# Kernel tuning notes

Hardware: AMD Instinct MI355X
Metric: run time of the kernel (lower is better)

Reference implementation:

```python
import jax, jax.numpy as jnp
import numpy as np

PI = 3.141592653589793
DET_THRESHOLD = 0.25
MAX_DET = 100
REG_HEAD = 4
DEPTH_MEAN = 28.01  # smoke_coder.depth_ref[0]
DIM_REF = (3.88, 1.63, 1.53)  # smoke_coder.dim_ref[0] (l, h, w)


def setup_inputs() -> dict:
    key = jax.random.key(0)
    k1, k2, k3, k4 = jax.random.split(key, 4)
    B, C, H, W = 32, 3, 256, 832  # stride-4 feature map of 3328x1024 images
    pred_heatmap = jax.random.uniform(k1, (B, C, H, W), dtype=jnp.float32)
    pred_regression = jax.random.normal(k2, (B, C + 1, H, W), dtype=jnp.float32) * 0.1  # REG_HEAD=4 channels
    trans_mat = jnp.tile(jnp.array([[0.25, 0.0, 0.0], [0.0, 0.25, 0.0], [0.0, 0.0, 1.0]], jnp.float32), (B, 1, 1))
    K_mat = jnp.tile(jnp.array([[2100.0, 0.0, 1664.0], [0.0, 2100.0, 512.0], [0.0, 0.0, 1.0]], jnp.float32), (B, 1, 1))
    size = jnp.tile(jnp.array([3328.0, 1024.0], jnp.float32), (B, 1))  # (img_w, img_h)
    h_cam = jax.random.uniform(k3, (B,), jnp.float32, 1.4, 2.0)
    dimensions = jax.random.uniform(k4, (B, 3), jnp.float32, 1.5, 4.0)
    return dict(pred_heatmap=pred_heatmap, pred_regression=pred_regression, trans_mat=trans_mat,
                K_mat=K_mat, size=size, h_cam=h_cam, dimensions=dimensions)


def reference(pred_heatmap, pred_regression, trans_mat, K_mat, size, h_cam, dimensions):
    B, C, H, W = pred_heatmap.shape
    K = MAX_DET
    # ---- nms_hm: 3x3 max-pool, keep local maxima ----
    hmax = jax.lax.reduce_window(pred_heatmap, -jnp.inf, jax.lax.max, (1, 1, 3, 3), (1, 1, 1, 1), 'SAME')
    heat = pred_heatmap * (hmax == pred_heatmap).astype(pred_heatmap.dtype)
    # ---- select_topk: per-class topk then global topk ----
    scores_c, inds_c = jax.lax.top_k(heat.reshape(B, C, H * W), K)  # [B,C,K]
    ys_c = (inds_c // W).astype(jnp.float32)
    xs_c = (inds_c % W).astype(jnp.float32)
    scores, topk_ind = jax.lax.top_k(scores_c.reshape(B, C * K), K)  # [B,K]
    clses = (topk_ind // K).astype(jnp.float32)
    inds = jnp.take_along_axis(inds_c.reshape(B, C * K), topk_ind, axis=1)
    ys = jnp.take_along_axis(ys_c.reshape(B, C * K), topk_ind, axis=1)
    xs = jnp.take_along_axis(xs_c.reshape(B, C * K), topk_ind, axis=1)
    feat = pred_regression.reshape(B, REG_HEAD, H * W).transpose(0, 2, 1)  # [B,HW,R]
    pois = jnp.take_along_axis(feat, inds[:, :, None], axis=1).reshape(-1, REG_HEAD)  # [B*K,R]
    log_dv_delta = pois[:, 0]
    off_u = pois[:, 1]
    ori = pois[:, 2:]
    # ---- feature points -> image points via inverse affine ----
    pts = jnp.stack([xs.reshape(-1), ys.reshape(-1)], axis=1)
    pts = pts + jnp.stack([off_u, jnp.zeros_like(off_u)], axis=1)
    pts_h = jnp.concatenate([pts, jnp.ones((pts.shape[0], 1), pts.dtype)], axis=1)  # [N,3]
    obj = jnp.repeat(jnp.arange(B), K)
    trans_inv = jnp.linalg.inv(trans_mat)[obj]  # [N,3,3]
    img_pts = jnp.einsum('nij,nj->ni', trans_inv, pts_h)[:, :2]
    # ---- per-object camera params ----
    Ks = K_mat[obj]
    h = h_cam[obj]
    kd = dimensions[obj]
    fx, fy, cx = Ks[:, 0, 0], Ks[:, 1, 1], Ks[:, 0, 2]
    dim_ref = jnp.array(DIM_REF, jnp.float32)
    dims = jnp.where(jnp.isfinite(kd), kd, dim_ref[None, :])
    # ---- geometric depth decode ----
    h_ref = h - dims[:, 1] / 2.0
    log_dv_ref = jnp.log(jnp.clip(fy * jnp.abs(h_ref), 1e-7, None) / DEPTH_MEAN)
    log_dv = jnp.clip(log_dv_ref + log_dv_delta, -4.0, 8.0)
    depths = jnp.clip(fy * jnp.abs(h_ref) * jnp.exp(-log_dv), 0.5, 120.0)
    px = (img_pts[:, 0] - cx) * depths / fx
    locs = jnp.stack([px, h, depths], axis=1)  # [N,3]
    # ---- decode_orientation (SMOKE) ----
    rays = jnp.arctan(locs[:, 0] / (locs[:, 2] + 1e-7))
    alphas = jnp.arctan(ori[:, 0] / (ori[:, 1] + 1e-7))
    alphas = alphas + jnp.where(ori[:, 1] >= 0, -PI / 2, PI / 2)
    rotys = alphas + rays
    rotys = jnp.where(rotys > PI, rotys - 2 * PI, rotys)
    rotys = jnp.where(rotys < -PI, rotys + 2 * PI, rotys)
    # ---- encode_box2d: build 3D corners, rotate, project, clamp ----
    cos, sin = jnp.cos(rotys), jnp.sin(rotys)
    cx8 = jnp.array([-0.5, 0.5, 0.5, 0.5, 0.5, -0.5, -0.5, -0.5], jnp.float32)
    cy8 = jnp.array([-1.0, -1.0, 0.0, 0.0, -1.0, -1.0, 0.0, 0.0], jnp.float32)
    cz8 = jnp.array([-0.5, -0.5, -0.5, 0.5, 0.5, 0.5, 0.5, -0.5], jnp.float32)
    xc = dims[:, 0:1] * cx8  # l
    yc = dims[:, 1:2] * cy8  # h
    zc = dims[:, 2:3] * cz8  # w
    bx = cos[:, None] * xc + sin[:, None] * zc
    bz = -sin[:, None] * xc + cos[:, None] * zc
    box3d = jnp.stack([bx, yc, bz], axis=1) + locs[:, :, None]  # [N,3,8]
    proj = jnp.einsum('nij,njk->nik', Ks, box3d)
    uv = proj[:, :2, :] / proj[:, 2:3, :]
    img_w = size.reshape(-1)[0]
    img_h = size.reshape(-1)[1]
    xmins = jnp.clip(jnp.min(uv[:, 0, :], axis=1), 0.0, img_w)
    xmaxs = jnp.clip(jnp.max(uv[:, 0, :], axis=1), 0.0, img_w)
    ymins = jnp.clip(jnp.min(uv[:, 1, :], axis=1), 0.0, img_h)
    ymaxs = jnp.clip(jnp.max(uv[:, 1, :], axis=1), 0.0, img_h)
    box2d = jnp.stack([xmins, ymins, xmaxs, ymaxs], axis=1)
    pred_dims = jnp.roll(dims, -1, axis=1)  # (l,h,w)->(h,w,l)
    result = jnp.concatenate([clses.reshape(-1, 1), alphas[:, None], box2d, pred_dims, locs,
                              rotys[:, None], scores.reshape(-1, 1)], axis=1)  # [N,14]
    # fixed-shape equivalent of boolean filtering: zero out rows below threshold
    keep = (result[:, -1] > DET_THRESHOLD).astype(result.dtype)
    return result * keep[:, None]
```

## Files before the change

### kernel.cpp

```cpp
#include <hip/hip_runtime.h>
#include <math.h>

#define B_ 32
#define C_ 3
#define H_ 256
#define W_ 832
#define HW_ (H_*W_)
#define K_ 100
#define RPB 16
#define PARTS (H_/RPB)
#define NLOAD (W_/4)
#define BLK 256
#define CAP 2048
#define NCAND (C_*PARTS*K_)
#define NB 2048
#define TIE_CAP 128
#define SEL_PASSES 6

typedef unsigned long long ull;

template<int N>
__device__ inline void bitonic_sort_desc(ull* s) {
    for (int k = 2; k <= N; k <<= 1) {
        for (int j = k >> 1; j > 0; j >>= 1) {
            __syncthreads();
            for (int i = threadIdx.x; i < N; i += BLK) {
                int ixj = i ^ j;
                if (ixj > i) {
                    ull a = s[i], b = s[ixj];
                    bool up = ((i & k) == 0);
                    if (up ? (a < b) : (a > b)) { s[i] = b; s[ixj] = a; }
                }
            }
        }
    }
    __syncthreads();
}

__device__ inline void find_digit(const unsigned* __restrict__ hist,
                                  unsigned* __restrict__ wtot,
                                  const int kneed,
                                  int* __restrict__ d_s,
                                  int* __restrict__ krem_s,
                                  int* __restrict__ m_s) {
    const int tid = threadIdx.x;
    const int lane = tid & 63;
    const int wid = tid >> 6;
    unsigned l[8];
    unsigned Ls = 0;
    #pragma unroll
    for (int j = 0; j < 8; ++j) { l[j] = hist[tid * 8 + j]; Ls += l[j]; }
    unsigned x = Ls;
    #pragma unroll
    for (int off = 1; off < 64; off <<= 1) {
        unsigned y = __shfl_down(x, off);
        if (lane + off < 64) x += y;
    }
    if (lane == 0) wtot[wid] = x;
    __syncthreads();
    unsigned tail = 0;
    #pragma unroll
    for (int w = 0; w < 4; ++w) if (w > wid) tail += wtot[w];
    unsigned s = x - Ls + tail;
    #pragma unroll
    for (int j = 7; j >= 0; --j) {
        const unsigned Sj = s + l[j];
        if (Sj >= (unsigned)kneed && s < (unsigned)kneed) {
            *d_s = tid * 8 + j;
            *krem_s = kneed - (int)s;
            *m_s = (int)l[j];
        }
        s = Sj;
    }
    __syncthreads();
}

__device__ inline void select_topk(const ull* __restrict__ buf, const int cnt,
                                   ull* __restrict__ dst,
                                   unsigned* __restrict__ hist,
                                   ull* __restrict__ tie,
                                   unsigned* __restrict__ wtot,
                                   int* __restrict__ sh) {
    const int tid = threadIdx.x;
    if (tid == 0) sh[0] = 0;
    int kneed = K_;
    int pshift = 0;
    ull prefix = 0;
    for (int pass = 0; pass < SEL_PASSES; ++pass) {
        const int rs = 53 - 11 * pass;
        const int shift = (rs > 0) ? rs : 0;
        #pragma unroll
        for (int j = 0; j < NB / BLK; ++j) hist[tid + j * BLK] = 0u;
        if (tid == 0) sh[1] = 0;
        __syncthreads();
        for (int i = tid; i < cnt; i += BLK) {
            const ull key = buf[i];
            if (pass > 0 && (key >> pshift) != prefix) continue;
            atomicAdd(&hist[(unsigned)(key >> shift) & 2047u], 1u);
        }
        __syncthreads();
        find_digit(hist, wtot, kneed, &sh[2], &sh[3], &sh[4]);
        const int d = sh[2], krem = sh[3], m = sh[4];
        const bool last = (m <= TIE_CAP) || (pass == SEL_PASSES - 1);
        for (int i = tid; i < cnt; i += BLK) {
            const ull key = buf[i];
            if (pass > 0 && (key >> pshift) != prefix) continue;
            const int dg = (int)((unsigned)(key >> shift) & 2047u);
            if (dg > d) {
                dst[atomicAdd(&sh[0], 1)] = key;
            } else if (last && dg == d) {
                const int p = atomicAdd(&sh[1], 1);
                if (p < TIE_CAP) tie[p] = key;
            }
        }
        __syncthreads();
        if (last) {
            const int n1 = K_ - krem;
            if (sh[1] <= TIE_CAP) {
                const int mm = sh[1];
                for (int i = tid; i < mm; i += BLK) {
                    const ull key = tie[i];
                    int r = 0;
                    for (int j = 0; j < mm; ++j) r += (tie[j] > key) ? 1 : 0;
                    if (r < krem) dst[n1 + r] = key;
                }
            } else {
                for (int i = tid; i < krem; i += BLK) dst[n1 + i] = tie[0];
            }
            __syncthreads();
            return;
        }
        prefix = (prefix << 11) | (ull)(unsigned)d;
        pshift = shift;
        kneed = krem;
    }
}

__global__ void __launch_bounds__(BLK) topk_part_kernel(
        const float* __restrict__ heat, ull* __restrict__ part_out) {
    const int chan = blockIdx.x / PARTS;
    const int c    = chan % C_;
    const int part = blockIdx.x % PARTS;
    const float* __restrict__ hp = heat + (size_t)chan * HW_;
    const int r0 = part * RPB;
    const int tid = threadIdx.x;
    const bool active = tid < NLOAD;
    const int x4 = tid * 4;
    const int lane = tid & 63;

    __shared__ unsigned hist[NB];
    __shared__ ull buf[CAP];
    __shared__ ull tie[TIE_CAP];
    __shared__ unsigned wtot[4];
    __shared__ int cnt;
    __shared__ int selsh[5];
    if (tid == 0) cnt = 0;

    const bool needL = active && (lane == 0) && (tid > 0);
    const bool needR = active && (lane == 63);

    float4 rA, rB, rC, rD;
    float aL = 0.f, bL = 0.f, cL = 0.f, dL = 0.f;
    float aR = 0.f, bR = 0.f, cR = 0.f, dR = 0.f;
    {
        const int ym1 = (r0 == 0) ? 0 : r0 - 1;
        const int yp1 = (r0 == H_ - 1) ? r0 : r0 + 1;
        if (active) {
            rA = reinterpret_cast<const float4*>(hp + (size_t)ym1 * W_)[tid];
            rB = reinterpret_cast<const float4*>(hp + (size_t)r0  * W_)[tid];
            rC = reinterpret_cast<const float4*>(hp + (size_t)yp1 * W_)[tid];
        }
        if (needL) {
            aL = hp[(size_t)ym1 * W_ + x4 - 1];
            bL = hp[(size_t)r0  * W_ + x4 - 1];
            cL = hp[(size_t)yp1 * W_ + x4 - 1];
        }
        if (needR) {
            aR = hp[(size_t)ym1 * W_ + x4 + 4];
            bR = hp[(size_t)r0  * W_ + x4 + 4];
            cR = hp[(size_t)yp1 * W_ + x4 + 4];
        }
    }
    __syncthreads();

    if (active) {
        for (int r = 0; r < RPB; ++r) {
            const int y = r0 + r;
            const int yn = (y + 2 > H_ - 1) ? H_ - 1 : y + 2;
            rD = reinterpret_cast<const float4*>(hp + (size_t)yn * W_)[tid];
            if (needL) dL = hp[(size_t)yn * W_ + x4 - 1];
            if (needR) dR = hp[(size_t)yn * W_ + x4 + 4];

            float4 vm;
            vm.x = fmaxf(fmaxf(rA.x, rB.x), rC.x);
            vm.y = fmaxf(fmaxf(rA.y, rB.y), rC.y);
            vm.z = fmaxf(fmaxf(rA.z, rB.z), rC.z);
            vm.w = fmaxf(fmaxf(rA.w, rB.w), rC.w);
            const float lmax = needL ? fmaxf(fmaxf(aL, bL), cL) : -INFINITY;
            const float rmax = needR ? fmaxf(fmaxf(aR, bR), cR) : -INFINITY;

            float left  = __shfl_up(vm.w, 1);
            float right = __shfl_down(vm.x, 1);
            if (lane == 0) left = lmax;
            if (lane == 63 || tid == NLOAD - 1) right = rmax;

            const float vn[6] = {left, vm.x, vm.y, vm.z, vm.w, right};
            const float vv[4] = {rB.x, rB.y, rB.z, rB.w};
            #pragma unroll
            for (int i = 0; i < 4; ++i) {
                const float v = vv[i];
                const bool peak = (v >= vn[i]) && (v >= vn[i+1]) && (v >= vn[i+2]);
                const ull m = __ballot(peak);
                if (peak) {
                    const unsigned p = (unsigned)(y * W_ + x4 + i);
                    const unsigned tiek = ((unsigned)c << 18) | p;
                    const ull key = ((ull)__float_as_uint(v) << 32) | (ull)(~tiek);
                    const int rank = __popcll(m & ((1ULL << lane) - 1ULL));
                    const int leader = __ffsll((long long)m) - 1;
                    int base = 0;
                    if (lane == leader) base = atomicAdd(&cnt, (int)__popcll(m));
                    base = __shfl(base, leader);
                    const int pos = base + rank;
                    if (pos < CAP) buf[pos] = key;
                }
            }
            rA = rB; rB = rC; rC = rD;
            aL = bL; bL = cL; cL = dL;
            aR = bR; bR = cR; cR = dR;
        }
    }
    __syncthreads();

    const int cc = (cnt < CAP) ? cnt : CAP;
    ull* o = part_out + (size_t)blockIdx.x * K_;

    if (cc <= K_) {
        for (int i = tid; i < cc; i += BLK) o[i] = buf[i];
        for (int i = cc + tid; i < K_; i += BLK) o[i] = 0ULL;
        return;
    }

    select_topk(buf, cc, o, hist, tie, wtot, selsh);
}

__global__ void __launch_bounds__(BLK) merge_geom_kernel(
        const ull* __restrict__ part_keys, const float* __restrict__ reg,
        const float* __restrict__ trans, const float* __restrict__ Km,
        const float* __restrict__ sz, const float* __restrict__ hcam,
        const float* __restrict__ dimen, float* __restrict__ out) {
    const int b = blockIdx.x;
    const int tid = threadIdx.x;
    __shared__ ull buf[NCAND];
    __shared__ unsigned hist[NB];
    __shared__ ull sel[128];
    __shared__ ull tie[TIE_CAP];
    __shared__ unsigned wtot[4];
    __shared__ int selsh[5];
    const ull* src = part_keys + (size_t)b * NCAND;
    for (int i = tid; i < NCAND; i += BLK) buf[i] = src[i];
    if (tid < 128) sel[tid] = 0ULL;
    __syncthreads();

    select_topk(buf, NCAND, sel, hist, tie, wtot, selsh);

    bitonic_sort_desc<128>(sel);

    for (int i = tid; i < K_; i += BLK) {
        const ull key = sel[i];
        const unsigned tiek = ~(unsigned)(key & 0xFFFFFFFFULL);
        const float score = __uint_as_float((unsigned)(key >> 32));
        const float clsf = (float)((tiek >> 18) & 3u);
        unsigned hw = tiek & 0x3FFFFu;
        if (hw >= HW_) hw = 0;
        const float xs = (float)(hw % W_);
        const float ys = (float)(hw / W_);

        const float* rg = reg + (size_t)b * 4 * HW_;
        const float delta = rg[hw];
        const float off_u = rg[HW_ + hw];
        const float ori0  = rg[2 * HW_ + hw];
        const float ori1  = rg[3 * HW_ + hw];

        const float* T = trans + b * 9;
        const float t00=T[0], t01=T[1], t02=T[2], t10=T[3], t11=T[4], t12=T[5],
                    t20=T[6], t21=T[7], t22=T[8];
        const float det3 = t00*(t11*t22 - t12*t21) - t01*(t10*t22 - t12*t20)
                         + t02*(t10*t21 - t11*t20);
        const float idt = 1.0f / det3;
        const float i00 = (t11*t22 - t12*t21)*idt;
        const float i01 = (t02*t21 - t01*t22)*idt;
        const float i02 = (t01*t12 - t02*t11)*idt;

        const float pu = xs + off_u;
        const float img_x = i00*pu + i01*ys + i02;

        const float* Kb = Km + b * 9;
        const float k00=Kb[0],k01=Kb[1],k02=Kb[2],k10=Kb[3],k11=Kb[4],k12=Kb[5],
                    k20=Kb[6],k21=Kb[7],k22=Kb[8];
        const float fx = k00, fy = k11, cx = k02;
        const float h = hcam[b];
        float d0 = dimen[b*3+0], d1 = dimen[b*3+1], d2 = dimen[b*3+2];
        if (!isfinite(d0)) d0 = 3.88f;
        if (!isfinite(d1)) d1 = 1.63f;
        if (!isfinite(d2)) d2 = 1.53f;

        const float h_ref = h - d1 * 0.5f;
        const float fyh = fy * fabsf(h_ref);
        const float log_dv_ref = logf(fmaxf(fyh, 1e-7f) / 28.01f);
        const float log_dv = fminf(fmaxf(log_dv_ref + delta, -4.0f), 8.0f);
        const float depth = fminf(fmaxf(fyh * expf(-log_dv), 0.5f), 120.0f);
        const float px = (img_x - cx) * depth / fx;

        const float PI_F  = 3.14159265358979323846f;
        const float ray = atanf(px / (depth + 1e-7f));
        float alpha = atanf(ori0 / (ori1 + 1e-7f));
        alpha += (ori1 >= 0.0f) ? -1.5707963267948966f : 1.5707963267948966f;
        float roty = alpha + ray;
        if (roty >  PI_F) roty -= 6.283185307179586f;
        if (roty < -PI_F) roty += 6.283185307179586f;

        const float cosr = cosf(roty), sinr = sinf(roty);
        const float cx8[8] = {-0.5f, 0.5f, 0.5f, 0.5f, 0.5f,-0.5f,-0.5f,-0.5f};
        const float cy8[8] = {-1.0f,-1.0f, 0.0f, 0.0f,-1.0f,-1.0f, 0.0f, 0.0f};
        const float cz8[8] = {-0.5f,-0.5f,-0.5f, 0.5f, 0.5f, 0.5f, 0.5f,-0.5f};
        float umin = 1e30f, umax = -1e30f, vmin = 1e30f, vmax = -1e30f;
        #pragma unroll
        for (int j = 0; j < 8; ++j) {
            const float xc = d0 * cx8[j];
            const float yc = d1 * cy8[j];
            const float zc = d2 * cz8[j];
            const float X = cosr*xc + sinr*zc + px;
            const float Y = yc + h;
            const float Z = -sinr*xc + cosr*zc + depth;
            const float w = k20*X + k21*Y + k22*Z;
            const float u = (k00*X + k01*Y + k02*Z) / w;
            const float v = (k10*X + k11*Y + k12*Z) / w;
            umin = fminf(umin, u); umax = fmaxf(umax, u);
            vmin = fminf(vmin, v); vmax = fmaxf(vmax, v);
        }
        const float img_w = sz[0], img_h = sz[1];
        const float xmin = fminf(fmaxf(umin, 0.0f), img_w);
        const float xmax = fminf(fmaxf(umax, 0.0f), img_w);
        const float ymin = fminf(fmaxf(vmin, 0.0f), img_h);
        const float ymax = fminf(fmaxf(vmax, 0.0f), img_h);

        const float keep = (score > 0.25f) ? 1.0f : 0.0f;
        float* o = out + (size_t)(b * K_ + i) * 14;
        o[0]  = clsf  * keep;
        o[1]  = alpha * keep;
        o[2]  = xmin  * keep;
        o[3]  = ymin  * keep;
        o[4]  = xmax  * keep;
        o[5]  = ymax  * keep;
        o[6]  = d1    * keep;
        o[7]  = d2    * keep;
        o[8]  = d0    * keep;
        o[9]  = px    * keep;
        o[10] = h     * keep;
        o[11] = depth * keep;
        o[12] = roty  * keep;
        o[13] = score * keep;
    }
}

extern "C" void kernel_launch(void* const* d_in, const int* in_sizes, int n_in,
                              void* d_out, int out_size, void* d_ws, size_t ws_size,
                              hipStream_t stream) {
    const float* heat  = (const float*)d_in[0];
    const float* reg   = (const float*)d_in[1];
    const float* trans = (const float*)d_in[2];
    const float* Kmat  = (const float*)d_in[3];
    const float* sz    = (const float*)d_in[4];
    const float* hcam  = (const float*)d_in[5];
    const float* dimen = (const float*)d_in[6];
    float* out = (float*)d_out;

    ull* part_keys = (ull*)d_ws;

    topk_part_kernel<<<B_ * C_ * PARTS, BLK, 0, stream>>>(heat, part_keys);
    merge_geom_kernel<<<B_, BLK, 0, stream>>>(
        part_keys, reg, trans, Kmat, sz, hcam, dimen, out);
}
```

Baseline: 241.4 us.

## Use overlapping wave halos, deeper row prefetch, and aggregated histogram atomics

The 3x3 NMS scan is restructured so that each wave covers 62 quads plus one ghost lane on each side. Neighbour columns then come from shuffles instead of extra scalar halo loads. Rows are kept in a six-deep register ring so that loads run further ahead, and the four per-column ballots are combined into a single atomicAdd per wave per row. The first radix-select pass now groups equal digits within a wave before each shared-memory atomic, to cut contention. In exchange, edge quads are loaded redundantly, more registers are used, and the leader-election loop costs extra when digits are diverse.

```diff
diff --git a/kernel.cpp b/kernel.cpp
--- a/kernel.cpp
+++ b/kernel.cpp
@@ -6,16 +6,17 @@
 #define H_ 256
 #define W_ 832
 #define HW_ (H_*W_)
+#define NQ (W_/4)
 #define K_ 100
 #define RPB 16
 #define PARTS (H_/RPB)
-#define NLOAD (W_/4)
 #define BLK 256
 #define CAP 2048
 #define NCAND (C_*PARTS*K_)
 #define NB 2048
 #define TIE_CAP 128
 #define SEL_PASSES 6
+#define QPW 62
 
 typedef unsigned long long ull;
 
@@ -82,6 +83,7 @@
                                    unsigned* __restrict__ wtot,
                                    int* __restrict__ sh) {
     const int tid = threadIdx.x;
+    const int lane = tid & 63;
     if (tid == 0) sh[0] = 0;
     int kneed = K_;
     int pshift = 0;
@@ -93,10 +95,25 @@
         for (int j = 0; j < NB / BLK; ++j) hist[tid + j * BLK] = 0u;
         if (tid == 0) sh[1] = 0;
         __syncthreads();
-        for (int i = tid; i < cnt; i += BLK) {
-            const ull key = buf[i];
-            if (pass > 0 && (key >> pshift) != prefix) continue;
-            atomicAdd(&hist[(unsigned)(key >> shift) & 2047u], 1u);
+        if (pass == 0) {
+            for (int i = tid; i < cnt; i += BLK) {
+                const unsigned dg = (unsigned)(buf[i] >> shift) & 2047u;
+                ull unclaimed = __ballot(1);
+                while (unclaimed) {
+                    const int leader = __ffsll((long long)unclaimed) - 1;
+                    const unsigned ldg = __shfl(dg, leader);
+                    const ull same = __ballot(dg == ldg);
+                    if (lane == leader)
+                        atomicAdd(&hist[ldg], (unsigned)__popcll(same));
+                    unclaimed &= ~same;
+                }
+            }
+        } else {
+            for (int i = tid; i < cnt; i += BLK) {
+                const ull key = buf[i];
+                if ((key >> pshift) != prefix) continue;
+                atomicAdd(&hist[(unsigned)(key >> shift) & 2047u], 1u);
+            }
         }
         __syncthreads();
         find_digit(hist, wtot, kneed, &sh[2], &sh[3], &sh[4]);
@@ -144,9 +161,13 @@
     const float* __restrict__ hp = heat + (size_t)chan * HW_;
     const int r0 = part * RPB;
     const int tid = threadIdx.x;
-    const bool active = tid < NLOAD;
-    const int x4 = tid * 4;
     const int lane = tid & 63;
+    const int wid = tid >> 6;
+
+    const int q = QPW * wid + lane - 1;
+    const bool ghost = (q < 0) || (q >= NQ);
+    const int qc = (q < 0) ? 0 : ((q >= NQ) ? NQ - 1 : q);
+    const bool emitter = (lane >= 1) && (lane <= QPW) && !ghost;
 
     __shared__ unsigned hist[NB];
     __shared__ ull buf[CAP];
@@ -156,77 +177,64 @@
     __shared__ int selsh[5];
     if (tid == 0) cnt = 0;
 
-    const bool needL = active && (lane == 0) && (tid > 0);
-    const bool needR = active && (lane == 63);
-
-    float4 rA, rB, rC, rD;
-    float aL = 0.f, bL = 0.f, cL = 0.f, dL = 0.f;
-    float aR = 0.f, bR = 0.f, cR = 0.f, dR = 0.f;
-    {
-        const int ym1 = (r0 == 0) ? 0 : r0 - 1;
-        const int yp1 = (r0 == H_ - 1) ? r0 : r0 + 1;
-        if (active) {
-            rA = reinterpret_cast<const float4*>(hp + (size_t)ym1 * W_)[tid];
-            rB = reinterpret_cast<const float4*>(hp + (size_t)r0  * W_)[tid];
-            rC = reinterpret_cast<const float4*>(hp + (size_t)yp1 * W_)[tid];
-        }
-        if (needL) {
-            aL = hp[(size_t)ym1 * W_ + x4 - 1];
-            bL = hp[(size_t)r0  * W_ + x4 - 1];
-            cL = hp[(size_t)yp1 * W_ + x4 - 1];
-        }
-        if (needR) {
-            aR = hp[(size_t)ym1 * W_ + x4 + 4];
-            bR = hp[(size_t)r0  * W_ + x4 + 4];
-            cR = hp[(size_t)yp1 * W_ + x4 + 4];
-        }
-    }
-    __syncthreads();
-
-    if (active) {
-        for (int r = 0; r < RPB; ++r) {
-            const int y = r0 + r;
-            const int yn = (y + 2 > H_ - 1) ? H_ - 1 : y + 2;
-            rD = reinterpret_cast<const float4*>(hp + (size_t)yn * W_)[tid];
-            if (needL) dL = hp[(size_t)yn * W_ + x4 - 1];
-            if (needR) dR = hp[(size_t)yn * W_ + x4 + 4];
-
-            float4 vm;
-            vm.x = fmaxf(fmaxf(rA.x, rB.x), rC.x);
-            vm.y = fmaxf(fmaxf(rA.y, rB.y), rC.y);
-            vm.z = fmaxf(fmaxf(rA.z, rB.z), rC.z);
-            vm.w = fmaxf(fmaxf(rA.w, rB.w), rC.w);
-            const float lmax = needL ? fmaxf(fmaxf(aL, bL), cL) : -INFINITY;
-            const float rmax = needR ? fmaxf(fmaxf(aR, bR), cR) : -INFINITY;
-
-            float left  = __shfl_up(vm.w, 1);
-            float right = __shfl_down(vm.x, 1);
-            if (lane == 0) left = lmax;
-            if (lane == 63 || tid == NLOAD - 1) right = rmax;
-
-            const float vn[6] = {left, vm.x, vm.y, vm.z, vm.w, right};
-            const float vv[4] = {rB.x, rB.y, rB.z, rB.w};
+    float4 R[6];
+    #pragma unroll
+    for (int j = 0; j < 6; ++j) {
+        int row = r0 - 1 + j;
+        row = (row < 0) ? 0 : ((row > H_ - 1) ? H_ - 1 : row);
+        R[j] = reinterpret_cast<const float4*>(hp + (size_t)row * W_)[qc];
+    }
+    __syncthreads();
+
+    #pragma unroll
+    for (int r = 0; r < RPB; ++r) {
+        const int y = r0 + r;
+        const float4 ra = R[r % 6];
+        const float4 rb = R[(r + 1) % 6];
+        const float4 rc = R[(r + 2) % 6];
+        if (r < RPB - 4) {
+            const int yn = (y + 5 > H_ - 1) ? H_ - 1 : y + 5;
+            R[r % 6] = reinterpret_cast<const float4*>(hp + (size_t)yn * W_)[qc];
+        }
+
+        float4 vm;
+        vm.x = fmaxf(fmaxf(ra.x, rb.x), rc.x);
+        vm.y = fmaxf(fmaxf(ra.y, rb.y), rc.y);
+        vm.z = fmaxf(fmaxf(ra.z, rb.z), rc.z);
+        vm.w = fmaxf(fmaxf(ra.w, rb.w), rc.w);
+        if (ghost) { vm.x = vm.y = vm.z = vm.w = -INFINITY; }
+
+        const float left  = __shfl_up(vm.w, 1);
+        const float right = __shfl_down(vm.x, 1);
+
+        const float vn[6] = {left, vm.x, vm.y, vm.z, vm.w, right};
+        const float vv[4] = {rb.x, rb.y, rb.z, rb.w};
+        ull m[4];
+        bool pk[4];
+        #pragma unroll
+        for (int i = 0; i < 4; ++i) {
+            pk[i] = emitter && (vv[i] >= vn[i]) && (vv[i] >= vn[i+1]) && (vv[i] >= vn[i+2]);
+            m[i] = __ballot(pk[i]);
+        }
+        const int tot = (int)(__popcll(m[0]) + __popcll(m[1]) +
+                              __popcll(m[2]) + __popcll(m[3]));
+        if (tot) {
+            int base = 0;
+            if (lane == 0) base = atomicAdd(&cnt, tot);
+            base = __shfl(base, 0);
+            int off = 0;
             #pragma unroll
             for (int i = 0; i < 4; ++i) {
-                const float v = vv[i];
-                const bool peak = (v >= vn[i]) && (v >= vn[i+1]) && (v >= vn[i+2]);
-                const ull m = __ballot(peak);
-                if (peak) {
-                    const unsigned p = (unsigned)(y * W_ + x4 + i);
+                if (pk[i]) {
+                    const unsigned p = (unsigned)(y * W_ + q * 4 + i);
                     const unsigned tiek = ((unsigned)c << 18) | p;
-                    const ull key = ((ull)__float_as_uint(v) << 32) | (ull)(~tiek);
-                    const int rank = __popcll(m & ((1ULL << lane) - 1ULL));
-                    const int leader = __ffsll((long long)m) - 1;
-                    int base = 0;
-                    if (lane == leader) base = atomicAdd(&cnt, (int)__popcll(m));
-                    base = __shfl(base, leader);
-                    const int pos = base + rank;
+                    const ull key = ((ull)__float_as_uint(vv[i]) << 32) | (ull)(~tiek);
+                    const int rank = (int)__popcll(m[i] & ((1ULL << lane) - 1ULL));
+                    const int pos = base + off + rank;
                     if (pos < CAP) buf[pos] = key;
                 }
-            }
-            rA = rB; rB = rC; rC = rD;
-            aL = bL; bL = cL; cL = dL;
-            aR = bR; bR = cR; cR = dR;
+                off += (int)__popcll(m[i]);
+            }
         }
     }
     __syncthreads();
```

Result: no change. 239.9 us (-0.6%).
